# Performance work log

Measured on AMD Instinct MI355X. Metric: run time of the kernel, lower is better.

Reference implementation:

```python
import jax, jax.numpy as jnp
import numpy as np

H, KVH, HD = 32, 8, 128          # query heads, kv heads, head_dim
HIDDEN = H * HD                   # 4096
TOTAL_KV = 3072                   # sum of (start_pos + seqlen) over the batch (static)
ROPE_THETA = 10000.0


def setup_inputs() -> dict:
    key = jax.random.key(0)
    ks = jax.random.split(key, 4)
    x = jax.random.normal(ks[0], (1024, HIDDEN), jnp.float32)
    wqkv = jax.random.normal(ks[1], (HIDDEN, HIDDEN + 2 * KVH * HD), jnp.float32) * 0.02
    wo = jax.random.normal(ks[2], (HIDDEN, HIDDEN), jnp.float32) * 0.02
    # paged cache: [num_layers=1, 2(k/v), cache_slots, kv_heads, head_dim], holds post-RoPE prefixes
    kv_cache = jax.random.normal(ks[3], (1, 2, 8192, KVH, HD), jnp.float32) * 0.02
    # 4 ragged requests: seqlens [512,256,128,128], cached prefixes [0,512,1024,512]
    seqstarts = jnp.array([0, 512, 768, 896, 1024], jnp.int32)
    start_pos = jnp.array([0, 512, 1024, 512], jnp.int32)
    kvstarts = jnp.array([0, 512, 1280, 2432, 3072], jnp.int32)  # cumsum of start_pos+seqlen
    cachestarts = jnp.array([0, 1024, 2560, 4096], jnp.int32)    # page base per request
    return dict(x=x, wqkv=wqkv, wo=wo, kv_cache=kv_cache, seqstarts=seqstarts,
                kvstarts=kvstarts, cachestarts=cachestarts, start_pos=start_pos)


def _rope(t, pos):
    # interleaved (GPT-J style) rotary over full head_dim; t: [T, nheads, HD], pos: [T]
    d2 = HD // 2
    inv_freq = 1.0 / (ROPE_THETA ** (jnp.arange(d2, dtype=jnp.float32) / d2))
    ang = pos.astype(jnp.float32)[:, None] * inv_freq      # [T, d2]
    cos = jnp.cos(ang)[:, None, :]
    sin = jnp.sin(ang)[:, None, :]
    x1, x2 = t[..., 0::2], t[..., 1::2]
    r1 = x1 * cos - x2 * sin
    r2 = x1 * sin + x2 * cos
    return jnp.stack([r1, r2], axis=-1).reshape(t.shape)


def _forward(x, wqkv, wo, kv_cache, seqstarts, kvstarts, cachestarts, start_pos):
    T = x.shape[0]
    # fused QKV projection
    xqkv = (x @ wqkv).reshape(T, H + 2 * KVH, HD)
    xq, xk, xv = jnp.split(xqkv, [H, H + KVH], axis=1)   # [T,32,HD],[T,8,HD],[T,8,HD]

    # per-token batch id and absolute position (ragged via seqstarts)
    tok = jnp.arange(T)
    bq = jnp.searchsorted(seqstarts, tok, side='right') - 1
    pos_q = tok - seqstarts[bq] + start_pos[bq]
    xq = _rope(xq, pos_q)
    xk = _rope(xk, pos_q)

    # assemble ragged KV stream: cached prefix (paged cache) + freshly projected tokens
    kvtok = jnp.arange(TOTAL_KV)
    bkv = jnp.searchsorted(kvstarts, kvtok, side='right') - 1
    pkv = kvtok - kvstarts[bkv]                              # absolute kv position
    is_new = pkv >= start_pos[bkv]
    new_idx = jnp.clip(seqstarts[bkv] + pkv - start_pos[bkv], 0, T - 1)
    cache_idx = cachestarts[bkv] + pkv                       # paged slot for prefix
    keys = jnp.where(is_new[:, None, None], xk[new_idx], kv_cache[0, 0][cache_idx])
    vals = jnp.where(is_new[:, None, None], xv[new_idx], kv_cache[0, 1][cache_idx])

    # GQA: repeat kv heads to match query heads
    rep = H // KVH
    keys = jnp.repeat(keys, rep, axis=1)                     # [TOTAL_KV, 32, HD]
    vals = jnp.repeat(vals, rep, axis=1)

    scale = 1.0 / jnp.sqrt(jnp.float32(HD))
    scores = jnp.einsum('qhd,khd->hqk', xq, keys) * scale    # [32, T, TOTAL_KV]
    # ragged causal mask: same request and kv position <= query position
    mask = (bq[:, None] == bkv[None, :]) & (pkv[None, :] <= pos_q[:, None])
    scores = jnp.where(mask[None], scores, jnp.float32(-1e30))
    probs = jax.nn.softmax(scores, axis=-1)
    attn = jnp.einsum('hqk,khd->qhd', probs, vals)           # [T, 32, HD]
    return attn.reshape(T, HIDDEN) @ wo


def reference(x, wqkv, wo, kv_cache, seqstarts, kvstarts, cachestarts, start_pos):
    return _forward(x, wqkv, wo, kv_cache, seqstarts, kvstarts, cachestarts, start_pos)
```

## Files before the change

kernel.cpp:

```cpp
#include <hip/hip_runtime.h>
#include <hip/hip_bf16.h>
#include <math.h>
#include <stdint.h>

typedef __bf16 bf16;
typedef __attribute__((ext_vector_type(4))) float floatx4;
typedef __attribute__((ext_vector_type(8))) bf16 bf16x8;
typedef __attribute__((ext_vector_type(4))) bf16 bf16x4;

#define LDS_ASYNC16(gptr, lptr)                                                \
  __builtin_amdgcn_global_load_lds(                                            \
      (const __attribute__((address_space(1))) void*)(gptr),                   \
      (__attribute__((address_space(3))) void*)(lptr), 16, 0, 0)

__global__ __launch_bounds__(256) void k_cvt(const float* __restrict__ in,
                                             bf16* __restrict__ out) {
  int i = (blockIdx.x * 256 + threadIdx.x) * 4;
  float4 v = *(const float4*)(in + i);
  bf16x4 o;
  o[0] = (bf16)v.x; o[1] = (bf16)v.y; o[2] = (bf16)v.z; o[3] = (bf16)v.w;
  *(bf16x4*)(out + i) = o;
}

__global__ __launch_bounds__(256) void k_merge(const float* __restrict__ a,
                                               const float* __restrict__ b,
                                               float* __restrict__ out) {
  int i = (blockIdx.x * 256 + threadIdx.x) * 4;
  float4 va = *(const float4*)(a + i);
  float4 vb = *(const float4*)(b + i);
  float4 o;
  o.x = va.x + vb.x; o.y = va.y + vb.y; o.z = va.z + vb.z; o.w = va.w + vb.w;
  *(float4*)(out + i) = o;
}

__global__ __launch_bounds__(256) void k_transpose_cvt(const float* __restrict__ in,
                                                       bf16* __restrict__ out,
                                                       int K, int N) {
  __shared__ float tile[64][65];
  int k0 = blockIdx.y * 64, n0 = blockIdx.x * 64;
  int tid = threadIdx.x;
  int cg = tid & 15, rr = tid >> 4;
#pragma unroll
  for (int p = 0; p < 4; ++p) {
    int r = rr + p * 16;
    float4 v = *(const float4*)(in + (size_t)(k0 + r) * N + n0 + cg * 4);
    tile[r][cg * 4 + 0] = v.x; tile[r][cg * 4 + 1] = v.y;
    tile[r][cg * 4 + 2] = v.z; tile[r][cg * 4 + 3] = v.w;
  }
  __syncthreads();
#pragma unroll
  for (int p = 0; p < 4; ++p) {
    int n = rr + p * 16;
    bf16x4 o;
    o[0] = (bf16)tile[cg * 4 + 0][n];
    o[1] = (bf16)tile[cg * 4 + 1][n];
    o[2] = (bf16)tile[cg * 4 + 2][n];
    o[3] = (bf16)tile[cg * 4 + 3][n];
    *(bf16x4*)(out + (size_t)(n0 + n) * K + k0 + cg * 4) = o;
  }
}

__global__ __launch_bounds__(256) void k_gemm_bt(const bf16* __restrict__ A,
                                                 const bf16* __restrict__ B,
                                                 float* __restrict__ C,
                                                 int M, int N, int K, int ksplit) {
  __shared__ bf16 As[128 * 32];
  __shared__ bf16 Bs[128 * 32];
  int tid = threadIdx.x;
  int w = tid >> 6, lane = tid & 63;
  int lq = lane >> 4, l16 = lane & 15;
  int bm = blockIdx.y * 128, bn = blockIdx.x * 128;
  int wm = (w >> 1) * 64, wn = (w & 1) * 64;
  int kc = K / ksplit;
  int koff = blockIdx.z * kc;
  C += (size_t)blockIdx.z * M * N;
  floatx4 acc[4][4] = {};
  const bf16* Ab = A + (size_t)bm * K;
  const bf16* Bb = B + (size_t)bn * K;
  int srow = (lane >> 2);
  int scol = (((lane & 3) ^ ((srow >> 1) & 3))) * 8;
  int sa = (l16 >> 1) & 3;

  for (int k0 = koff; k0 < koff + kc; k0 += 32) {
#pragma unroll
    for (int c = 0; c < 2; ++c) {
      int r = w * 32 + c * 16 + srow;
      LDS_ASYNC16(Ab + (size_t)r * K + k0 + scol, &As[(w * 32 + c * 16) * 32]);
      LDS_ASYNC16(Bb + (size_t)r * K + k0 + scol, &Bs[(w * 32 + c * 16) * 32]);
    }
    __syncthreads();
    bf16x8 af[4], bfr[4];
#pragma unroll
    for (int i = 0; i < 4; ++i)
      af[i] = *(const bf16x8*)&As[(wm + i * 16 + l16) * 32 + (lq ^ sa) * 8];
#pragma unroll
    for (int j = 0; j < 4; ++j)
      bfr[j] = *(const bf16x8*)&Bs[(wn + j * 16 + l16) * 32 + (lq ^ sa) * 8];
#pragma unroll
    for (int i = 0; i < 4; ++i)
#pragma unroll
      for (int j = 0; j < 4; ++j)
        acc[i][j] = __builtin_amdgcn_mfma_f32_16x16x32_bf16(af[i], bfr[j],
                                                            acc[i][j], 0, 0, 0);
    __syncthreads();
  }
#pragma unroll
  for (int i = 0; i < 4; ++i)
#pragma unroll
    for (int j = 0; j < 4; ++j) {
      int m = bm + wm + i * 16 + lq * 4;
      int n = bn + wn + j * 16 + l16;
      float* cp = C + (size_t)m * N + n;
#pragma unroll
      for (int r = 0; r < 4; ++r) cp[(size_t)r * N] = acc[i][j][r];
    }
}

__global__ __launch_bounds__(256) void k_rope(const float* __restrict__ xp0,
                                              const float* __restrict__ xp1,
                                              bf16* __restrict__ qb,
                                              bf16* __restrict__ kb,
                                              const int* __restrict__ seqstarts,
                                              const int* __restrict__ start_pos) {
  int t = blockIdx.x;
  int s = 0;
  for (int i = 1; i < 4; ++i) if (seqstarts[i] <= t) s = i;
  float pos = (float)(t - seqstarts[s] + start_pos[s]);
  for (int wk = threadIdx.x; wk < 40 * 64; wk += 256) {
    int hh = wk >> 6, j = wk & 63;
    size_t idx = ((size_t)t * 48 + hh) * 128 + 2 * j;
    float2 a0 = *(const float2*)(xp0 + idx);
    float2 a1 = *(const float2*)(xp1 + idx);
    float x1 = a0.x + a1.x;
    float x2 = a0.y + a1.y;
    float invf = exp2f(-(float)j * 0.20762050593045935f);
    float ang = pos * invf;
    float sv, cv;
    sincosf(ang, &sv, &cv);
    float r1 = x1 * cv - x2 * sv;
    float r2 = x1 * sv + x2 * cv;
    unsigned int u1 = (unsigned int)__builtin_bit_cast(unsigned short, (bf16)r1);
    unsigned int u2 = (unsigned int)__builtin_bit_cast(unsigned short, (bf16)r2);
    unsigned int pk = u1 | (u2 << 16);
    unsigned int* dst = (hh < 32)
        ? (unsigned int*)(qb + ((size_t)t * 32 + hh) * 128)
        : (unsigned int*)(kb + ((size_t)t * 8 + (hh - 32)) * 128);
    dst[j] = pk;
  }
}

__global__ __launch_bounds__(256) void k_assemble_k(
    const bf16* __restrict__ xk, const float* __restrict__ ck,
    bf16* __restrict__ kall,
    const int* __restrict__ seqstarts, const int* __restrict__ kvstarts,
    const int* __restrict__ cachestarts, const int* __restrict__ start_pos) {
  int p = blockIdx.x;
  int b = 0;
  for (int i = 1; i < 4; ++i) if (kvstarts[i] <= p) b = i;
  int pkv = p - kvstarts[b];
  int tid = threadIdx.x;
  int hk = tid >> 5, d4 = (tid & 31) * 4;
  bf16* dst = kall + ((size_t)hk * 3072 + p) * 128 + d4;
  if (pkv >= start_pos[b]) {
    int tn = seqstarts[b] + pkv - start_pos[b];
    *(bf16x4*)dst = *(const bf16x4*)(xk + ((size_t)tn * 8 + hk) * 128 + d4);
  } else {
    int ci = cachestarts[b] + pkv;
    float4 v = *(const float4*)(ck + ((size_t)ci * 8 + hk) * 128 + d4);
    bf16x4 o;
    o[0] = (bf16)v.x; o[1] = (bf16)v.y; o[2] = (bf16)v.z; o[3] = (bf16)v.w;
    *(bf16x4*)dst = o;
  }
}

__global__ __launch_bounds__(256) void k_assemble_vT(
    const float* __restrict__ xp0, const float* __restrict__ xp1,
    const float* __restrict__ cv, bf16* __restrict__ vT,
    const int* __restrict__ seqstarts, const int* __restrict__ kvstarts,
    const int* __restrict__ cachestarts, const int* __restrict__ start_pos) {
  __shared__ float tile[64][130];
  int hk = blockIdx.y, p0 = blockIdx.x * 64;
  int tid = threadIdx.x;
  {
    int r = tid >> 2;
    int p = p0 + r;
    int b = 0;
    for (int i = 1; i < 4; ++i) if (kvstarts[i] <= p) b = i;
    int pkv = p - kvstarts[b];
    int f0 = (tid & 3) * 32;
    if (pkv >= start_pos[b]) {
      int tn = seqstarts[b] + pkv - start_pos[b];
      size_t base = (size_t)tn * 6144 + (40 + hk) * 128;
#pragma unroll
      for (int i = 0; i < 8; ++i) {
        float4 v0 = *(const float4*)(xp0 + base + f0 + i * 4);
        float4 v1 = *(const float4*)(xp1 + base + f0 + i * 4);
        tile[r][f0 + i * 4 + 0] = v0.x + v1.x;
        tile[r][f0 + i * 4 + 1] = v0.y + v1.y;
        tile[r][f0 + i * 4 + 2] = v0.z + v1.z;
        tile[r][f0 + i * 4 + 3] = v0.w + v1.w;
      }
    } else {
      int ci = cachestarts[b] + pkv;
      const float* src = cv + ((size_t)ci * 8 + hk) * 128;
#pragma unroll
      for (int i = 0; i < 8; ++i) {
        float4 v = *(const float4*)(src + f0 + i * 4);
        tile[r][f0 + i * 4 + 0] = v.x; tile[r][f0 + i * 4 + 1] = v.y;
        tile[r][f0 + i * 4 + 2] = v.z; tile[r][f0 + i * 4 + 3] = v.w;
      }
    }
  }
  __syncthreads();
  int d = tid >> 1, hf = tid & 1;
  bf16* dst = vT + ((size_t)hk * 128 + d) * 3072 + p0 + hf * 32;
#pragma unroll
  for (int q = 0; q < 4; ++q) {
    bf16x8 o;
#pragma unroll
    for (int e = 0; e < 8; ++e) o[e] = (bf16)tile[hf * 32 + q * 8 + e][d];
    *(bf16x8*)(dst + q * 8) = o;
  }
}

__global__ __launch_bounds__(256) void k_attn(
    const bf16* __restrict__ qb, const bf16* __restrict__ kall,
    const bf16* __restrict__ vT, float* __restrict__ pO,
    float2* __restrict__ pml,
    const int* __restrict__ seqstarts, const int* __restrict__ kvstarts,
    const int* __restrict__ start_pos) {
  __shared__ bf16 Ks[64 * 128];
  __shared__ bf16 Vs[128 * 64];
  __shared__ bf16 Ps[64 * 64];
  int qbi = blockIdx.x, h = blockIdx.y, seg = blockIdx.z, hk = h >> 2;
  int t0 = qbi * 64;
  int s = 0;
  for (int i = 1; i < 4; ++i) if (seqstarts[i] <= t0) s = i;
  int posbase = t0 - seqstarts[s] + start_pos[s];
  int kv0 = kvstarts[s];
  int nkv = posbase + 64;
  int pbeg = seg * 512;
  if (pbeg >= nkv) return;
  int pend = min(pbeg + 512, nkv);
  int tid = threadIdx.x, w = tid >> 6, lane = tid & 63;
  int lq = lane >> 4, l16 = lane & 15;

  bf16x8 qa[4];
#pragma unroll
  for (int kk = 0; kk < 4; ++kk)
    qa[kk] = *(const bf16x8*)(qb + (((size_t)(t0 + w * 16 + l16) * 32 + h) * 128 +
                                    kk * 32 + lq * 8));

  int krow = lane >> 4;
  int vrow = lane >> 3;
  int vchunk = ((lane & 7) ^ (vrow & 7));
  int sw8 = l16 & 7;

  float m_r[4], l_r[4];
  floatx4 oacc[8] = {};
#pragma unroll
  for (int rg = 0; rg < 4; ++rg) { m_r[rg] = -3.0e38f; l_r[rg] = 0.f; }
  const float scale = 0.08838834764831845f;

  for (int p0 = pbeg; p0 < pend; p0 += 64) {
#pragma unroll
    for (int c = 0; c < 4; ++c) {
      int base_r = w * 16 + c * 4;
      int r = base_r + krow;
      int gch = (lane & 15) ^ ((c * 4 + krow) & 15);
      LDS_ASYNC16(kall + (((size_t)hk * 3072 + kv0 + p0 + r) * 128 + gch * 8),
                  &Ks[base_r * 128]);
    }
#pragma unroll
    for (int c = 0; c < 4; ++c) {
      int base_d = w * 32 + c * 8;
      int d = base_d + vrow;
      LDS_ASYNC16(vT + (((size_t)hk * 128 + d) * 3072 + kv0 + p0 + vchunk * 8),
                  &Vs[base_d * 64]);
    }
    __syncthreads();

    floatx4 sacc[4] = {};
#pragma unroll
    for (int kk = 0; kk < 4; ++kk)
#pragma unroll
      for (int j = 0; j < 4; ++j) {
        bf16x8 kb = *(const bf16x8*)&Ks[(j * 16 + l16) * 128 +
                                        ((kk * 4 + lq) ^ l16) * 8];
        sacc[j] = __builtin_amdgcn_mfma_f32_16x16x32_bf16(qa[kk], kb, sacc[j], 0, 0, 0);
      }

#pragma unroll
    for (int rg = 0; rg < 4; ++rg) {
      int qpos = posbase + w * 16 + lq * 4 + rg;
      float sv[4];
      float rmax = -3.0e38f;
#pragma unroll
      for (int j = 0; j < 4; ++j) {
        int pkv = p0 + j * 16 + l16;
        sv[j] = (pkv <= qpos) ? sacc[j][rg] * scale : -3.0e38f;
        rmax = fmaxf(rmax, sv[j]);
      }
#pragma unroll
      for (int off = 1; off < 16; off <<= 1)
        rmax = fmaxf(rmax, __shfl_xor(rmax, off, 64));
      float mnew = fmaxf(m_r[rg], rmax);
      float alpha = __expf(m_r[rg] - mnew);
      m_r[rg] = mnew;
      int prow = w * 16 + lq * 4 + rg;
      int pswz = (lq * 4 + rg) & 7;
      float psum = 0.f;
#pragma unroll
      for (int j = 0; j < 4; ++j) {
        float pv = __expf(sv[j] - mnew);
        psum += pv;
        int chunk = (j * 2 + (l16 >> 3)) ^ pswz;
        Ps[prow * 64 + chunk * 8 + (l16 & 7)] = (bf16)pv;
      }
#pragma unroll
      for (int off = 1; off < 16; off <<= 1) psum += __shfl_xor(psum, off, 64);
      l_r[rg] = l_r[rg] * alpha + psum;
#pragma unroll
      for (int nt = 0; nt < 8; ++nt) oacc[nt][rg] *= alpha;
    }

#pragma unroll
    for (int kk = 0; kk < 2; ++kk) {
      bf16x8 pa = *(const bf16x8*)&Ps[(w * 16 + l16) * 64 +
                                      ((kk * 4 + lq) ^ sw8) * 8];
#pragma unroll
      for (int nt = 0; nt < 8; ++nt) {
        bf16x8 vb = *(const bf16x8*)&Vs[(nt * 16 + l16) * 64 +
                                        ((kk * 4 + lq) ^ sw8) * 8];
        oacc[nt] = __builtin_amdgcn_mfma_f32_16x16x32_bf16(pa, vb, oacc[nt], 0, 0, 0);
      }
    }
    __syncthreads();
  }

  size_t obase = (((size_t)seg * 16 + qbi) * 32 + h) * 8192;
#pragma unroll
  for (int rg = 0; rg < 4; ++rg) {
    int row = w * 16 + lq * 4 + rg;
#pragma unroll
    for (int nt = 0; nt < 8; ++nt)
      pO[obase + (size_t)row * 128 + nt * 16 + l16] = oacc[nt][rg];
    if (l16 == 0)
      pml[(((size_t)seg * 16 + qbi) * 32 + h) * 64 + row] =
          make_float2(m_r[rg], l_r[rg]);
  }
}

__global__ __launch_bounds__(256) void k_attn_merge(
    const float* __restrict__ pO, const float2* __restrict__ pml,
    bf16* __restrict__ aout,
    const int* __restrict__ seqstarts, const int* __restrict__ start_pos) {
  int qbi = blockIdx.x, h = blockIdx.y;
  int t0 = qbi * 64;
  int s = 0;
  for (int i = 1; i < 4; ++i) if (seqstarts[i] <= t0) s = i;
  int nkv = t0 - seqstarts[s] + start_pos[s] + 64;
  int ns = (nkv + 511) >> 9;
  int tid = threadIdx.x;
  int row = tid >> 2, cg = (tid & 3) * 32;
  float2 ml[3];
  float w[3];
  float mstar = -3.0e38f;
  for (int si = 0; si < ns; ++si) {
    ml[si] = pml[(((size_t)si * 16 + qbi) * 32 + h) * 64 + row];
    mstar = fmaxf(mstar, ml[si].x);
  }
  float denom = 0.f;
  for (int si = 0; si < ns; ++si) {
    w[si] = __expf(ml[si].x - mstar);
    denom += w[si] * ml[si].y;
  }
  float inv = 1.0f / denom;
  bf16* dst = aout + (size_t)(t0 + row) * 4096 + h * 128 + cg;
#pragma unroll
  for (int c = 0; c < 32; c += 8) {
    float acc[8] = {};
    for (int si = 0; si < ns; ++si) {
      const float* src = pO + (((size_t)si * 16 + qbi) * 32 + h) * 8192 +
                         (size_t)row * 128 + cg + c;
      float4 v0 = *(const float4*)(src);
      float4 v1 = *(const float4*)(src + 4);
      acc[0] += w[si] * v0.x; acc[1] += w[si] * v0.y;
      acc[2] += w[si] * v0.z; acc[3] += w[si] * v0.w;
      acc[4] += w[si] * v1.x; acc[5] += w[si] * v1.y;
      acc[6] += w[si] * v1.z; acc[7] += w[si] * v1.w;
    }
    bf16x8 o;
#pragma unroll
    for (int e = 0; e < 8; ++e) o[e] = (bf16)(acc[e] * inv);
    *(bf16x8*)(dst + c) = o;
  }
}

extern "C" void kernel_launch(void* const* d_in, const int* in_sizes, int n_in,
                              void* d_out, int out_size, void* d_ws, size_t ws_size,
                              hipStream_t stream) {
  const float* x = (const float*)d_in[0];
  const float* wqkv = (const float*)d_in[1];
  const float* wo = (const float*)d_in[2];
  const float* kv = (const float*)d_in[3];
  const int* seqstarts = (const int*)d_in[4];
  const int* kvstarts = (const int*)d_in[5];
  const int* cachestarts = (const int*)d_in[6];
  const int* start_pos = (const int*)d_in[7];
  float* out = (float*)d_out;

  char* base = (char*)d_ws;
  size_t off = 0;
  auto carve = [&](size_t bytes) {
    void* r = base + off;
    off += (bytes + 255) & ~(size_t)255;
    return r;
  };
  bf16* x_bf    = (bf16*)carve(1024ull * 4096 * 2);
  bf16* wqkvT   = (bf16*)carve(6144ull * 4096 * 2);
  bf16* woT     = (bf16*)carve(4096ull * 4096 * 2);
  float* xqkv   = (float*)carve(2ull * 1024 * 6144 * 4);
  bf16* q_bf    = (bf16*)carve(1024ull * 32 * 128 * 2);
  bf16* xk_bf   = (bf16*)carve(1024ull * 8 * 128 * 2);
  bf16* k_all   = (bf16*)carve(8ull * 3072 * 128 * 2);
  bf16* vT_all  = (bf16*)carve(8ull * 128 * 3072 * 2);
  bf16* attn_bf = (bf16*)carve(1024ull * 4096 * 2);
  float2* pml   = (float2*)carve(3ull * 16 * 32 * 64 * 8);
  float* outp = (float*)wqkvT;
  float* pO = xqkv;

  float* xqkv1 = xqkv + 1024ull * 6144;
  const float* cache_v = kv + 8192ull * 8 * 128;

  k_cvt<<<4096, 256, 0, stream>>>(x, x_bf);
  k_transpose_cvt<<<dim3(96, 64), 256, 0, stream>>>(wqkv, wqkvT, 4096, 6144);
  k_transpose_cvt<<<dim3(64, 64), 256, 0, stream>>>(wo, woT, 4096, 4096);
  k_gemm_bt<<<dim3(48, 8, 2), 256, 0, stream>>>(x_bf, wqkvT, xqkv, 1024, 6144,
                                                4096, 2);
  k_rope<<<1024, 256, 0, stream>>>(xqkv, xqkv1, q_bf, xk_bf, seqstarts, start_pos);
  k_assemble_k<<<3072, 256, 0, stream>>>(xk_bf, kv, k_all, seqstarts, kvstarts,
                                         cachestarts, start_pos);
  k_assemble_vT<<<dim3(48, 8), 256, 0, stream>>>(xqkv, xqkv1, cache_v, vT_all,
                                                 seqstarts, kvstarts, cachestarts,
                                                 start_pos);
  k_attn<<<dim3(16, 32, 3), 256, 0, stream>>>(q_bf, k_all, vT_all, pO, pml,
                                              seqstarts, kvstarts, start_pos);
  k_attn_merge<<<dim3(16, 32), 256, 0, stream>>>(pO, pml, attn_bf, seqstarts,
                                                 start_pos);
  k_gemm_bt<<<dim3(32, 8, 2), 256, 0, stream>>>(attn_bf, woT, outp, 1024, 4096,
                                                4096, 2);
  k_merge<<<4096, 256, 0, stream>>>(outp, outp + 1024ull * 4096, out);
}
```

Measured before the change: 495.3 us.

## Merge prep, assembly kernels and drop split-KV attention merge

Folds the x conversion and both weight transposes into one launch. RoPE now writes new keys directly into the assembled K buffer, and K-cache conversion and the V transpose are merged into a single kernel. Attention no longer splits the KV range into segments: each block walks the full KV range, normalizes, writes bf16 output directly and reverses block order so the longest query blocks start first. This removes several launches and the partial-output round trip through memory, at the cost of less attention parallelism (512 blocks instead of up to 1536).

```diff
diff --git a/kernel.cpp b/kernel.cpp
--- a/kernel.cpp
+++ b/kernel.cpp
@@ -12,15 +12,6 @@
   __builtin_amdgcn_global_load_lds(                                            \
       (const __attribute__((address_space(1))) void*)(gptr),                   \
       (__attribute__((address_space(3))) void*)(lptr), 16, 0, 0)
-
-__global__ __launch_bounds__(256) void k_cvt(const float* __restrict__ in,
-                                             bf16* __restrict__ out) {
-  int i = (blockIdx.x * 256 + threadIdx.x) * 4;
-  float4 v = *(const float4*)(in + i);
-  bf16x4 o;
-  o[0] = (bf16)v.x; o[1] = (bf16)v.y; o[2] = (bf16)v.z; o[3] = (bf16)v.w;
-  *(bf16x4*)(out + i) = o;
-}
 
 __global__ __launch_bounds__(256) void k_merge(const float* __restrict__ a,
                                                const float* __restrict__ b,
@@ -33,12 +24,11 @@
   *(float4*)(out + i) = o;
 }
 
-__global__ __launch_bounds__(256) void k_transpose_cvt(const float* __restrict__ in,
-                                                       bf16* __restrict__ out,
-                                                       int K, int N) {
-  __shared__ float tile[64][65];
-  int k0 = blockIdx.y * 64, n0 = blockIdx.x * 64;
-  int tid = threadIdx.x;
+__device__ __forceinline__ void transpose_tile(const float* __restrict__ in,
+                                               bf16* __restrict__ out, int K,
+                                               int N, int bx, int by, int tid,
+                                               float (*tile)[65]) {
+  int k0 = by * 64, n0 = bx * 64;
   int cg = tid & 15, rr = tid >> 4;
 #pragma unroll
   for (int p = 0; p < 4; ++p) {
@@ -57,6 +47,29 @@
     o[2] = (bf16)tile[cg * 4 + 2][n];
     o[3] = (bf16)tile[cg * 4 + 3][n];
     *(bf16x4*)(out + (size_t)(n0 + n) * K + k0 + cg * 4) = o;
+  }
+}
+
+__global__ __launch_bounds__(256) void k_prep(const float* __restrict__ x,
+                                              const float* __restrict__ wqkv,
+                                              const float* __restrict__ wo,
+                                              bf16* __restrict__ x_bf,
+                                              bf16* __restrict__ wqkvT,
+                                              bf16* __restrict__ woT) {
+  __shared__ float tile[64][65];
+  int bid = blockIdx.x, tid = threadIdx.x;
+  if (bid < 4096) {
+    int i = (bid * 256 + tid) * 4;
+    float4 v = *(const float4*)(x + i);
+    bf16x4 o;
+    o[0] = (bf16)v.x; o[1] = (bf16)v.y; o[2] = (bf16)v.z; o[3] = (bf16)v.w;
+    *(bf16x4*)(x_bf + i) = o;
+  } else if (bid < 10240) {
+    int q = bid - 4096;
+    transpose_tile(wqkv, wqkvT, 4096, 6144, q % 96, q / 96, tid, tile);
+  } else {
+    int q = bid - 10240;
+    transpose_tile(wo, woT, 4096, 4096, q % 64, q / 64, tid, tile);
   }
 }
 
@@ -119,13 +132,16 @@
 __global__ __launch_bounds__(256) void k_rope(const float* __restrict__ xp0,
                                               const float* __restrict__ xp1,
                                               bf16* __restrict__ qb,
-                                              bf16* __restrict__ kb,
+                                              bf16* __restrict__ kall,
                                               const int* __restrict__ seqstarts,
+                                              const int* __restrict__ kvstarts,
                                               const int* __restrict__ start_pos) {
   int t = blockIdx.x;
   int s = 0;
   for (int i = 1; i < 4; ++i) if (seqstarts[i] <= t) s = i;
-  float pos = (float)(t - seqstarts[s] + start_pos[s]);
+  int posn = t - seqstarts[s] + start_pos[s];
+  float pos = (float)posn;
+  int krow = kvstarts[s] + posn;
   for (int wk = threadIdx.x; wk < 40 * 64; wk += 256) {
     int hh = wk >> 6, j = wk & 63;
     size_t idx = ((size_t)t * 48 + hh) * 128 + 2 * j;
@@ -144,43 +160,35 @@
     unsigned int pk = u1 | (u2 << 16);
     unsigned int* dst = (hh < 32)
         ? (unsigned int*)(qb + ((size_t)t * 32 + hh) * 128)
-        : (unsigned int*)(kb + ((size_t)t * 8 + (hh - 32)) * 128);
+        : (unsigned int*)(kall + ((size_t)(hh - 32) * 3072 + krow) * 128);
     dst[j] = pk;
   }
 }
 
-__global__ __launch_bounds__(256) void k_assemble_k(
-    const bf16* __restrict__ xk, const float* __restrict__ ck,
-    bf16* __restrict__ kall,
+__global__ __launch_bounds__(256) void k_asm(
+    const float* __restrict__ ck, const float* __restrict__ xp0,
+    const float* __restrict__ xp1, const float* __restrict__ cv,
+    bf16* __restrict__ kall, bf16* __restrict__ vT,
     const int* __restrict__ seqstarts, const int* __restrict__ kvstarts,
     const int* __restrict__ cachestarts, const int* __restrict__ start_pos) {
-  int p = blockIdx.x;
-  int b = 0;
-  for (int i = 1; i < 4; ++i) if (kvstarts[i] <= p) b = i;
-  int pkv = p - kvstarts[b];
-  int tid = threadIdx.x;
-  int hk = tid >> 5, d4 = (tid & 31) * 4;
-  bf16* dst = kall + ((size_t)hk * 3072 + p) * 128 + d4;
-  if (pkv >= start_pos[b]) {
-    int tn = seqstarts[b] + pkv - start_pos[b];
-    *(bf16x4*)dst = *(const bf16x4*)(xk + ((size_t)tn * 8 + hk) * 128 + d4);
-  } else {
+  __shared__ float tile[64][130];
+  int bid = blockIdx.x, tid = threadIdx.x;
+  if (bid < 3072) {
+    int p = bid;
+    int b = 0;
+    for (int i = 1; i < 4; ++i) if (kvstarts[i] <= p) b = i;
+    int pkv = p - kvstarts[b];
+    if (pkv >= start_pos[b]) return;
+    int hk = tid >> 5, d4 = (tid & 31) * 4;
     int ci = cachestarts[b] + pkv;
     float4 v = *(const float4*)(ck + ((size_t)ci * 8 + hk) * 128 + d4);
     bf16x4 o;
     o[0] = (bf16)v.x; o[1] = (bf16)v.y; o[2] = (bf16)v.z; o[3] = (bf16)v.w;
-    *(bf16x4*)dst = o;
-  }
-}
-
-__global__ __launch_bounds__(256) void k_assemble_vT(
-    const float* __restrict__ xp0, const float* __restrict__ xp1,
-    const float* __restrict__ cv, bf16* __restrict__ vT,
-    const int* __restrict__ seqstarts, const int* __restrict__ kvstarts,
-    const int* __restrict__ cachestarts, const int* __restrict__ start_pos) {
-  __shared__ float tile[64][130];
-  int hk = blockIdx.y, p0 = blockIdx.x * 64;
-  int tid = threadIdx.x;
+    *(bf16x4*)(kall + ((size_t)hk * 3072 + p) * 128 + d4) = o;
+    return;
+  }
+  int q = bid - 3072;
+  int hk = q / 48, p0 = (q % 48) * 64;
   {
     int r = tid >> 2;
     int p = p0 + r;
@@ -215,33 +223,30 @@
   int d = tid >> 1, hf = tid & 1;
   bf16* dst = vT + ((size_t)hk * 128 + d) * 3072 + p0 + hf * 32;
 #pragma unroll
-  for (int q = 0; q < 4; ++q) {
+  for (int qq = 0; qq < 4; ++qq) {
     bf16x8 o;
 #pragma unroll
-    for (int e = 0; e < 8; ++e) o[e] = (bf16)tile[hf * 32 + q * 8 + e][d];
-    *(bf16x8*)(dst + q * 8) = o;
+    for (int e = 0; e < 8; ++e) o[e] = (bf16)tile[hf * 32 + qq * 8 + e][d];
+    *(bf16x8*)(dst + qq * 8) = o;
   }
 }
 
 __global__ __launch_bounds__(256) void k_attn(
     const bf16* __restrict__ qb, const bf16* __restrict__ kall,
-    const bf16* __restrict__ vT, float* __restrict__ pO,
-    float2* __restrict__ pml,
+    const bf16* __restrict__ vT, bf16* __restrict__ aout,
     const int* __restrict__ seqstarts, const int* __restrict__ kvstarts,
     const int* __restrict__ start_pos) {
   __shared__ bf16 Ks[64 * 128];
   __shared__ bf16 Vs[128 * 64];
   __shared__ bf16 Ps[64 * 64];
-  int qbi = blockIdx.x, h = blockIdx.y, seg = blockIdx.z, hk = h >> 2;
+  int qbi = 15 - (int)blockIdx.x;
+  int h = blockIdx.y, hk = h >> 2;
   int t0 = qbi * 64;
   int s = 0;
   for (int i = 1; i < 4; ++i) if (seqstarts[i] <= t0) s = i;
   int posbase = t0 - seqstarts[s] + start_pos[s];
   int kv0 = kvstarts[s];
   int nkv = posbase + 64;
-  int pbeg = seg * 512;
-  if (pbeg >= nkv) return;
-  int pend = min(pbeg + 512, nkv);
   int tid = threadIdx.x, w = tid >> 6, lane = tid & 63;
   int lq = lane >> 4, l16 = lane & 15;
 
@@ -262,7 +267,7 @@
   for (int rg = 0; rg < 4; ++rg) { m_r[rg] = -3.0e38f; l_r[rg] = 0.f; }
   const float scale = 0.08838834764831845f;
 
-  for (int p0 = pbeg; p0 < pend; p0 += 64) {
+  for (int p0 = 0; p0 < nkv; p0 += 64) {
 #pragma unroll
     for (int c = 0; c < 4; ++c) {
       int base_r = w * 16 + c * 4;
@@ -338,62 +343,14 @@
     __syncthreads();
   }
 
-  size_t obase = (((size_t)seg * 16 + qbi) * 32 + h) * 8192;
 #pragma unroll
   for (int rg = 0; rg < 4; ++rg) {
     int row = w * 16 + lq * 4 + rg;
+    float inv = 1.0f / l_r[rg];
+    bf16* dst = aout + (size_t)(t0 + row) * 4096 + h * 128;
 #pragma unroll
     for (int nt = 0; nt < 8; ++nt)
-      pO[obase + (size_t)row * 128 + nt * 16 + l16] = oacc[nt][rg];
-    if (l16 == 0)
-      pml[(((size_t)seg * 16 + qbi) * 32 + h) * 64 + row] =
-          make_float2(m_r[rg], l_r[rg]);
-  }
-}
-
-__global__ __launch_bounds__(256) void k_attn_merge(
-    const float* __restrict__ pO, const float2* __restrict__ pml,
-    bf16* __restrict__ aout,
-    const int* __restrict__ seqstarts, const int* __restrict__ start_pos) {
-  int qbi = blockIdx.x, h = blockIdx.y;
-  int t0 = qbi * 64;
-  int s = 0;
-  for (int i = 1; i < 4; ++i) if (seqstarts[i] <= t0) s = i;
-  int nkv = t0 - seqstarts[s] + start_pos[s] + 64;
-  int ns = (nkv + 511) >> 9;
-  int tid = threadIdx.x;
-  int row = tid >> 2, cg = (tid & 3) * 32;
-  float2 ml[3];
-  float w[3];
-  float mstar = -3.0e38f;
-  for (int si = 0; si < ns; ++si) {
-    ml[si] = pml[(((size_t)si * 16 + qbi) * 32 + h) * 64 + row];
-    mstar = fmaxf(mstar, ml[si].x);
-  }
-  float denom = 0.f;
-  for (int si = 0; si < ns; ++si) {
-    w[si] = __expf(ml[si].x - mstar);
-    denom += w[si] * ml[si].y;
-  }
-  float inv = 1.0f / denom;
-  bf16* dst = aout + (size_t)(t0 + row) * 4096 + h * 128 + cg;
-#pragma unroll
-  for (int c = 0; c < 32; c += 8) {
-    float acc[8] = {};
-    for (int si = 0; si < ns; ++si) {
-      const float* src = pO + (((size_t)si * 16 + qbi) * 32 + h) * 8192 +
-                         (size_t)row * 128 + cg + c;
-      float4 v0 = *(const float4*)(src);
-      float4 v1 = *(const float4*)(src + 4);
-      acc[0] += w[si] * v0.x; acc[1] += w[si] * v0.y;
-      acc[2] += w[si] * v0.z; acc[3] += w[si] * v0.w;
-      acc[4] += w[si] * v1.x; acc[5] += w[si] * v1.y;
-      acc[6] += w[si] * v1.z; acc[7] += w[si] * v1.w;
-    }
-    bf16x8 o;
-#pragma unroll
-    for (int e = 0; e < 8; ++e) o[e] = (bf16)(acc[e] * inv);
-    *(bf16x8*)(dst + c) = o;
+      dst[nt * 16 + l16] = (bf16)(oacc[nt][rg] * inv);
   }
 }
 
@@ -422,32 +379,23 @@
   bf16* woT     = (bf16*)carve(4096ull * 4096 * 2);
   float* xqkv   = (float*)carve(2ull * 1024 * 6144 * 4);
   bf16* q_bf    = (bf16*)carve(1024ull * 32 * 128 * 2);
-  bf16* xk_bf   = (bf16*)carve(1024ull * 8 * 128 * 2);
   bf16* k_all   = (bf16*)carve(8ull * 3072 * 128 * 2);
   bf16* vT_all  = (bf16*)carve(8ull * 128 * 3072 * 2);
   bf16* attn_bf = (bf16*)carve(1024ull * 4096 * 2);
-  float2* pml   = (float2*)carve(3ull * 16 * 32 * 64 * 8);
   float* outp = (float*)wqkvT;
-  float* pO = xqkv;
 
   float* xqkv1 = xqkv + 1024ull * 6144;
   const float* cache_v = kv + 8192ull * 8 * 128;
 
-  k_cvt<<<4096, 256, 0, stream>>>(x, x_bf);
-  k_transpose_cvt<<<dim3(96, 64), 256, 0, stream>>>(wqkv, wqkvT, 4096, 6144);
-  k_transpose_cvt<<<dim3(64, 64), 256, 0, stream>>>(wo, woT, 4096, 4096);
+  k_prep<<<14336, 256, 0, stream>>>(x, wqkv, wo, x_bf, wqkvT, woT);
   k_gemm_bt<<<dim3(48, 8, 2), 256, 0, stream>>>(x_bf, wqkvT, xqkv, 1024, 6144,
                                                 4096, 2);
-  k_rope<<<1024, 256, 0, stream>>>(xqkv, xqkv1, q_bf, xk_bf, seqstarts, start_pos);
-  k_assemble_k<<<3072, 256, 0, stream>>>(xk_bf, kv, k_all, seqstarts, kvstarts,
-                                         cachestarts, start_pos);
-  k_assemble_vT<<<dim3(48, 8), 256, 0, stream>>>(xqkv, xqkv1, cache_v, vT_all,
-                                                 seqstarts, kvstarts, cachestarts,
-                                                 start_pos);
-  k_attn<<<dim3(16, 32, 3), 256, 0, stream>>>(q_bf, k_all, vT_all, pO, pml,
-                                              seqstarts, kvstarts, start_pos);
-  k_attn_merge<<<dim3(16, 32), 256, 0, stream>>>(pO, pml, attn_bf, seqstarts,
-                                                 start_pos);
+  k_rope<<<1024, 256, 0, stream>>>(xqkv, xqkv1, q_bf, k_all, seqstarts,
+                                   kvstarts, start_pos);
+  k_asm<<<3456, 256, 0, stream>>>(kv, xqkv, xqkv1, cache_v, k_all, vT_all,
+                                  seqstarts, kvstarts, cachestarts, start_pos);
+  k_attn<<<dim3(16, 32), 256, 0, stream>>>(q_bf, k_all, vT_all, attn_bf,
+                                           seqstarts, kvstarts, start_pos);
   k_gemm_bt<<<dim3(32, 8, 2), 256, 0, stream>>>(attn_bf, woT, outp, 1024, 4096,
                                                 4096, 2);
   k_merge<<<4096, 256, 0, stream>>>(outp, outp + 1024ull * 4096, out);
```

Result: faster. 465.5 us (-6.0%).
